# Kernel optimization log

Hardware: AMD Instinct MI355X
Metric: run time of the kernel (lower is better)

Reference implementation:

```python
import jax, jax.numpy as jnp
import numpy as np

EMBED = 1024
HEADS = 16
HEAD_DIM = EMBED // HEADS
B, S = 8, 1024


def setup_inputs() -> dict:
    key = jax.random.key(0)
    ks = jax.random.split(key, 9)
    sd = 0.02
    return {
        "x": jax.random.normal(ks[0], (B, S, EMBED), dtype=jnp.float32),
        "wq": jax.random.normal(ks[1], (EMBED, EMBED), dtype=jnp.float32) * sd,
        "bq": jnp.zeros((EMBED,), dtype=jnp.float32),
        "wk": jax.random.normal(ks[2], (EMBED, EMBED), dtype=jnp.float32) * sd,
        "bk": jnp.zeros((EMBED,), dtype=jnp.float32),
        "wv": jax.random.normal(ks[3], (EMBED, EMBED), dtype=jnp.float32) * sd,
        "bv": jnp.zeros((EMBED,), dtype=jnp.float32),
        "wo": jax.random.normal(ks[4], (EMBED, EMBED), dtype=jnp.float32) * sd,
        "bo": jnp.zeros((EMBED,), dtype=jnp.float32),
    }


def reference(x, wq, bq, wk, bk, wv, bv, wo, bo):
    b, s, e = x.shape
    scale = HEAD_DIM ** -0.5
    # projections (torch Linear: x @ W^T + b)
    q = x @ wq.T + bq
    k = x @ wk.T + bk
    v = x @ wv.T + bv
    # [b, h, s, d]
    q = q.reshape(b, s, HEADS, HEAD_DIM).transpose(0, 2, 1, 3)
    k = k.reshape(b, s, HEADS, HEAD_DIM).transpose(0, 2, 1, 3)
    v = v.reshape(b, s, HEADS, HEAD_DIM).transpose(0, 2, 1, 3)
    scores = jnp.einsum("bhqd,bhkd->bhqk", q, k) * scale
    probs = jax.nn.softmax(scores, axis=-1)
    out = jnp.einsum("bhqk,bhkd->bhqd", probs, v)
    out = out.transpose(0, 2, 1, 3).reshape(b, s, e)
    return out @ wo.T + bo
```

## Files before the change

### kernel.cpp

```cpp
#include <hip/hip_runtime.h>
#include <hip/hip_bf16.h>
#include <math.h>

#define EMBED 1024
#define HEADS 16
#define HDIM 64
#define BATCH 8
#define SEQL 1024
#define MROWS (BATCH * SEQL)

typedef _Float16 f16x8 __attribute__((ext_vector_type(8)));
typedef float    f32x4 __attribute__((ext_vector_type(4)));

__device__ __forceinline__ void gload_lds16(const void* g, void* l) {
    __builtin_amdgcn_global_load_lds(
        (__attribute__((address_space(1))) void*)g,
        (__attribute__((address_space(3))) void*)l, 16, 0, 0);
}

__device__ __forceinline__ unsigned pack_f16(float a, float b) {
    union { _Float16 h[2]; unsigned u; } t;
    t.h[0] = (_Float16)a; t.h[1] = (_Float16)b;
    return t.u;
}

__global__ __launch_bounds__(256)
void cvt_f16(const float* __restrict__ in, _Float16* __restrict__ out)
{
    const int r = blockIdx.x;
    const int c4 = threadIdx.x * 4;
    const float4 v = *reinterpret_cast<const float4*>(&in[(size_t)r * EMBED + c4]);
    union { _Float16 h[4]; short4 s; } u;
    u.h[0] = (_Float16)v.x; u.h[1] = (_Float16)v.y;
    u.h[2] = (_Float16)v.z; u.h[3] = (_Float16)v.w;
    *reinterpret_cast<short4*>(out + (size_t)r * EMBED + c4) = u.s;
}

__global__ __launch_bounds__(256)
void cvt_w4(const float* __restrict__ wq, const float* __restrict__ wk,
            const float* __restrict__ wv, const float* __restrict__ wo,
            _Float16* __restrict__ out)
{
    const int bid  = blockIdx.x;
    const int wsel = bid >> 10;
    const int row  = bid & 1023;
    const float* in = (wsel == 0) ? wq : (wsel == 1) ? wk : (wsel == 2) ? wv : wo;
    const int c4 = threadIdx.x * 4;
    const float4 v = *reinterpret_cast<const float4*>(&in[(size_t)row * EMBED + c4]);
    union { _Float16 h[4]; short4 s; } u;
    u.h[0] = (_Float16)v.x; u.h[1] = (_Float16)v.y;
    u.h[2] = (_Float16)v.z; u.h[3] = (_Float16)v.w;
    *reinterpret_cast<short4*>(out + (size_t)bid * EMBED + c4) = u.s;
}

#define GN EMBED
#define BK 64

template <int MODE>
__global__ __launch_bounds__(256)
void gemm_mfma(const _Float16* __restrict__ A, const _Float16* __restrict__ B,
               const float* __restrict__ bias, void* __restrict__ Cout,
               float scale)
{
    __shared__ __align__(16) _Float16 As[128][BK];
    __shared__ __align__(16) _Float16 Bs[128][BK];

    const int bid = blockIdx.x;
    const int xcd = bid & 7;
    const int idx = bid >> 3;
    const int bm  = (xcd * 8 + (idx >> 3)) * 128;
    const int bn  = (idx & 7) * 128;

    const int tid = threadIdx.x;
    const int w    = tid >> 6;
    const int lane = tid & 63;
    const int lr = lane & 15;
    const int lh = lane >> 4;
    const int wr = w >> 1;
    const int wc = w & 1;

    f32x4 acc[4][4];
    #pragma unroll
    for (int m = 0; m < 4; ++m)
        #pragma unroll
        for (int n = 0; n < 4; ++n) acc[m][n] = (f32x4){0.f, 0.f, 0.f, 0.f};

    for (int step = 0; step < 16; ++step) {
        const int kbase = step * BK;

        #pragma unroll
        for (int i = 0; i < 4; ++i) {
            const int idx2 = tid + i * 256;
            const int r    = idx2 >> 3;
            const int kc   = (idx2 & 7) * 8;
            gload_lds16(A + (size_t)(bm + r) * EMBED + kbase + kc,
                        (char*)As + i * 4096 + w * 1024);
            gload_lds16(B + (size_t)(bn + r) * EMBED + kbase + kc,
                        (char*)Bs + i * 4096 + w * 1024);
        }
        __syncthreads();

        #pragma unroll
        for (int kk = 0; kk < 2; ++kk) {
            f16x8 af[4], bfr[4];
            #pragma unroll
            for (int m = 0; m < 4; ++m)
                af[m] = *reinterpret_cast<const f16x8*>(
                    &As[wr * 64 + m * 16 + lr][kk * 32 + lh * 8]);
            #pragma unroll
            for (int n = 0; n < 4; ++n)
                bfr[n] = *reinterpret_cast<const f16x8*>(
                    &Bs[wc * 64 + n * 16 + lr][kk * 32 + lh * 8]);
            #pragma unroll
            for (int m = 0; m < 4; ++m)
                #pragma unroll
                for (int n = 0; n < 4; ++n)
                    acc[m][n] = __builtin_amdgcn_mfma_f32_16x16x32_f16(
                        af[m], bfr[n], acc[m][n], 0, 0, 0);
        }
        __syncthreads();
    }

    #pragma unroll
    for (int m = 0; m < 4; ++m) {
        #pragma unroll
        for (int n = 0; n < 4; ++n) {
            const int col = bn + wc * 64 + n * 16 + lr;
            const float bv = bias[col];
            #pragma unroll
            for (int j = 0; j < 4; ++j) {
                const int row = bm + wr * 64 + m * 16 + lh * 4 + j;
                const float f = acc[m][n][j] + bv;
                if (MODE == 0) {
                    ((float*)Cout)[(size_t)row * GN + col] = f;
                } else {
                    const int b = row >> 10, s = row & 1023;
                    const int h = col >> 6,  d = col & 63;
                    if (MODE == 2) {
                        ((_Float16*)Cout)[((size_t)(b * HEADS + h) * HDIM + d) * SEQL + s] =
                            (_Float16)f;
                    } else {
                        ((_Float16*)Cout)[((size_t)(b * HEADS + h) * SEQL + s) * HDIM + d] =
                            (_Float16)(f * scale);
                    }
                }
            }
        }
    }
}

#define KT 64

__global__ __launch_bounds__(512, 8)
void attn_mfma(const _Float16* __restrict__ Q2, const _Float16* __restrict__ K2,
               const _Float16* __restrict__ VT, _Float16* __restrict__ Ab)
{
    __shared__ __align__(16) char KVs[2][2][8192];

    const int bid = blockIdx.x;
    const int xcd = bid & 7;
    const int idx = bid >> 3;
    const int bh  = xcd * 16 + (idx >> 3);
    const int qt0 = (idx & 7) * 128;

    const int tid  = threadIdx.x;
    const int w    = tid >> 6;
    const int lane = tid & 63;
    const int lr = lane & 15;
    const int lh = lane >> 4;
    const int b   = bh >> 4;

    const _Float16* Qg = Q2 + (size_t)bh * SEQL * 64;
    const _Float16* Kg = K2 + (size_t)bh * SEQL * 64;
    const _Float16* Vg = VT + (size_t)bh * HDIM * SEQL;

    f16x8 qf[2];
    {
        const _Float16* qrow = Qg + (size_t)(qt0 + w * 16 + lr) * 64 + lh * 8;
        qf[0] = *reinterpret_cast<const f16x8*>(qrow);
        qf[1] = *reinterpret_cast<const f16x8*>(qrow + 32);
    }

    f32x4 oacc[4];
    #pragma unroll
    for (int nd = 0; nd < 4; ++nd) oacc[nd] = (f32x4){0.f, 0.f, 0.f, 0.f};
    float l_run = 0.f;

    const int s0 = lr + 32 * (lh & 1);
    const int s1 = s0 + 16;
    const bool hi_n = (lh >> 1) != 0;

#define STAGE(bufi, ktv) do {                                                  \
        const int r_  = tid >> 3;                                              \
        const int cb_ = ((tid & 7) * 16) ^ ((r_ & 7) << 4);                    \
        gload_lds16(Kg + (size_t)((ktv) * KT + r_) * 64 + cb_ / 2,             \
                    &KVs[bufi][0][w * 1024]);                                  \
        gload_lds16(Vg + (size_t)r_ * SEQL + (ktv) * KT + cb_ / 2,             \
                    &KVs[bufi][1][w * 1024]);                                  \
    } while (0)

    STAGE(0, 0);
    __syncthreads();

    for (int kt = 0; kt < SEQL / KT; ++kt) {
        if (kt < 15) STAGE((kt + 1) & 1, kt + 1);

        const char* Kb = (const char*)KVs[kt & 1][0];
        const char* Vb = (const char*)KVs[kt & 1][1];

        f32x4 sc[4];
        __builtin_amdgcn_s_setprio(1);
        #pragma unroll
        for (int n = 0; n < 4; ++n) {
            const int row = n * 16 + lr;
            const int o0 = row * 128 + ((lh * 16) ^ ((row & 7) << 4));
            const int o1 = row * 128 + ((64 + lh * 16) ^ ((row & 7) << 4));
            const f16x8 kf0 = *reinterpret_cast<const f16x8*>(Kb + o0);
            const f16x8 kf1 = *reinterpret_cast<const f16x8*>(Kb + o1);
            f32x4 s = (f32x4){0.f, 0.f, 0.f, 0.f};
            s = __builtin_amdgcn_mfma_f32_16x16x32_f16(kf0, qf[0], s, 0, 0, 0);
            s = __builtin_amdgcn_mfma_f32_16x16x32_f16(kf1, qf[1], s, 0, 0, 0);
            sc[n] = s;
        }
        __builtin_amdgcn_s_setprio(0);

        float p[4][4];
        float psn[4];
        #pragma unroll
        for (int n = 0; n < 4; ++n) {
            #pragma unroll
            for (int j = 0; j < 4; ++j)
                p[n][j] = exp2f(sc[n][j]);
            psn[n] = (p[n][0] + p[n][1]) + (p[n][2] + p[n][3]);
        }
        l_run += (psn[0] + psn[1]) + (psn[2] + psn[3]);

        unsigned pk[4][2];
        #pragma unroll
        for (int n = 0; n < 4; ++n) {
            pk[n][0] = pack_f16(p[n][0], p[n][1]);
            pk[n][1] = pack_f16(p[n][2], p[n][3]);
        }

        unsigned pa[2][4];
        #pragma unroll
        for (int ks = 0; ks < 2; ++ks) {
            const unsigned a0 = __shfl(pk[2 * ks][0],     s0);
            const unsigned b0 = __shfl(pk[2 * ks + 1][0], s0);
            const unsigned a1 = __shfl(pk[2 * ks][1],     s0);
            const unsigned b1 = __shfl(pk[2 * ks + 1][1], s0);
            const unsigned a2 = __shfl(pk[2 * ks][0],     s1);
            const unsigned b2 = __shfl(pk[2 * ks + 1][0], s1);
            const unsigned a3 = __shfl(pk[2 * ks][1],     s1);
            const unsigned b3 = __shfl(pk[2 * ks + 1][1], s1);
            pa[ks][0] = hi_n ? b0 : a0;
            pa[ks][1] = hi_n ? b1 : a1;
            pa[ks][2] = hi_n ? b2 : a2;
            pa[ks][3] = hi_n ? b3 : a3;
        }

        __builtin_amdgcn_s_setprio(1);
        #pragma unroll
        for (int ks = 0; ks < 2; ++ks) {
            const f16x8 pf = *reinterpret_cast<const f16x8*>(&pa[ks][0]);
            #pragma unroll
            for (int nd = 0; nd < 4; ++nd) {
                const int row = nd * 16 + lr;
                const int off = row * 128 +
                    ((ks * 64 + lh * 16) ^ ((row & 7) << 4));
                const f16x8 vf = *reinterpret_cast<const f16x8*>(Vb + off);
                oacc[nd] = __builtin_amdgcn_mfma_f32_16x16x32_f16(
                    pf, vf, oacc[nd], 0, 0, 0);
            }
        }
        __builtin_amdgcn_s_setprio(0);

        __syncthreads();
    }
#undef STAGE

    l_run += __shfl_xor(l_run, 16);
    l_run += __shfl_xor(l_run, 32);

    const int h = bh & (HEADS - 1);
    #pragma unroll
    for (int j = 0; j < 4; ++j) {
        const float lv = __shfl(l_run, (lane & 48) | ((4 * lh + j) & 15));
        const float rl = 1.f / lv;
        const size_t gm = (size_t)b * SEQL + qt0 + w * 16 + 4 * lh + j;
        #pragma unroll
        for (int nd = 0; nd < 4; ++nd) {
            const int e = h * 64 + nd * 16 + lr;
            Ab[gm * EMBED + e] = (_Float16)(oacc[nd][j] * rl);
        }
    }
}

extern "C" void kernel_launch(void* const* d_in, const int* in_sizes, int n_in,
                              void* d_out, int out_size, void* d_ws, size_t ws_size,
                              hipStream_t stream)
{
    const float* x  = (const float*)d_in[0];
    const float* wq = (const float*)d_in[1];
    const float* bq = (const float*)d_in[2];
    const float* wk = (const float*)d_in[3];
    const float* bk = (const float*)d_in[4];
    const float* wv = (const float*)d_in[5];
    const float* bv = (const float*)d_in[6];
    const float* wo = (const float*)d_in[7];
    const float* bo = (const float*)d_in[8];
    float* out = (float*)d_out;

    char* p = (char*)d_ws;
    _Float16* x2  = (_Float16*)p;  p += (size_t)MROWS * EMBED * 2;
    _Float16* wq2 = (_Float16*)p;  p += (size_t)EMBED * EMBED * 2;
    _Float16* wk2 = (_Float16*)p;  p += (size_t)EMBED * EMBED * 2;
    _Float16* wv2 = (_Float16*)p;  p += (size_t)EMBED * EMBED * 2;
    _Float16* wo2 = (_Float16*)p;  p += (size_t)EMBED * EMBED * 2;
    _Float16* Q2  = (_Float16*)p;  p += (size_t)BATCH * HEADS * SEQL * 64 * 2;
    _Float16* K2  = (_Float16*)p;  p += (size_t)BATCH * HEADS * SEQL * 64 * 2;
    _Float16* VT  = (_Float16*)p;  p += (size_t)BATCH * HEADS * HDIM * SEQL * 2;
    _Float16* Ab  = x2;

    const dim3 blk(256);
    cvt_f16<<<dim3(MROWS), blk, 0, stream>>>(x, x2);
    cvt_w4<<<dim3(4096), blk, 0, stream>>>(wq, wk, wv, wo, wq2);

    const float qscale = 0.125f * 1.4426950408889634f;
    gemm_mfma<3><<<dim3(512), blk, 0, stream>>>(x2, wq2, bq, Q2, qscale);
    gemm_mfma<3><<<dim3(512), blk, 0, stream>>>(x2, wk2, bk, K2, 1.0f);
    gemm_mfma<2><<<dim3(512), blk, 0, stream>>>(x2, wv2, bv, VT, 1.0f);

    attn_mfma<<<dim3(1024), dim3(512), 0, stream>>>(Q2, K2, VT, Ab);

    gemm_mfma<0><<<dim3(512), blk, 0, stream>>>(Ab, wo2, bo, out, 1.0f);
}
```

Measured before the change: 196.6 us.

## Fuse Q and K projections into one GEMM and unroll attention loop by two

Q and K projections now run as a single GEMM with N=2048, relying on wq2 and wk2 being contiguous in the workspace, and the epilogue routes columns to the Q or K buffer with per-projection bias and scale. The attention kernel unrolls its K/V loop by two with fixed double-buffer indices, precomputes swizzled LDS offsets and staging pointers outside the loop, and uses the packed cvt_pkrtz instruction for the f16 conversion. The aim is to remove one kernel launch and tail, give the projection GEMM a larger grid, and reduce per-iteration address arithmetic. The packed conversion rounds toward zero instead of to nearest, which slightly changes the probability values.

```diff
diff --git a/kernel.cpp b/kernel.cpp
--- a/kernel.cpp
+++ b/kernel.cpp
@@ -10,6 +10,7 @@
 #define MROWS (BATCH * SEQL)
 
 typedef _Float16 f16x8 __attribute__((ext_vector_type(8)));
+typedef __fp16   fp16x2 __attribute__((ext_vector_type(2)));
 typedef float    f32x4 __attribute__((ext_vector_type(4)));
 
 __device__ __forceinline__ void gload_lds16(const void* g, void* l) {
@@ -19,8 +20,8 @@
 }
 
 __device__ __forceinline__ unsigned pack_f16(float a, float b) {
-    union { _Float16 h[2]; unsigned u; } t;
-    t.h[0] = (_Float16)a; t.h[1] = (_Float16)b;
+    union { fp16x2 h; unsigned u; } t;
+    t.h = __builtin_amdgcn_cvt_pkrtz(a, b);
     return t.u;
 }
 
@@ -56,11 +57,11 @@
 #define GN EMBED
 #define BK 64
 
-template <int MODE>
+template <int MODE, int NBLK>
 __global__ __launch_bounds__(256)
 void gemm_mfma(const _Float16* __restrict__ A, const _Float16* __restrict__ B,
-               const float* __restrict__ bias, void* __restrict__ Cout,
-               float scale)
+               const float* __restrict__ bias, const float* __restrict__ bias2,
+               void* __restrict__ Cout, float scale)
 {
     __shared__ __align__(16) _Float16 As[128][BK];
     __shared__ __align__(16) _Float16 Bs[128][BK];
@@ -68,8 +69,8 @@
     const int bid = blockIdx.x;
     const int xcd = bid & 7;
     const int idx = bid >> 3;
-    const int bm  = (xcd * 8 + (idx >> 3)) * 128;
-    const int bn  = (idx & 7) * 128;
+    const int bm  = (xcd * 8 + (idx / NBLK)) * 128;
+    const int bn  = (idx % NBLK) * 128;
 
     const int tid = threadIdx.x;
     const int w    = tid >> 6;
@@ -126,7 +127,9 @@
         #pragma unroll
         for (int n = 0; n < 4; ++n) {
             const int col = bn + wc * 64 + n * 16 + lr;
-            const float bv = bias[col];
+            const int c   = col & 1023;
+            const int proj = col >> 10;
+            const float bv = (MODE == 4 && proj) ? bias2[c] : bias[c];
             #pragma unroll
             for (int j = 0; j < 4; ++j) {
                 const int row = bm + wr * 64 + m * 16 + lh * 4 + j;
@@ -135,13 +138,15 @@
                     ((float*)Cout)[(size_t)row * GN + col] = f;
                 } else {
                     const int b = row >> 10, s = row & 1023;
-                    const int h = col >> 6,  d = col & 63;
+                    const int h = c >> 6,  d = c & 63;
                     if (MODE == 2) {
                         ((_Float16*)Cout)[((size_t)(b * HEADS + h) * HDIM + d) * SEQL + s] =
                             (_Float16)f;
                     } else {
-                        ((_Float16*)Cout)[((size_t)(b * HEADS + h) * SEQL + s) * HDIM + d] =
-                            (_Float16)(f * scale);
+                        const float sc_ = proj ? 1.0f : scale;
+                        ((_Float16*)Cout)[(size_t)proj * MROWS * EMBED +
+                            ((size_t)(b * HEADS + h) * SEQL + s) * 64 + d] =
+                            (_Float16)(f * sc_);
                     }
                 }
             }
@@ -171,8 +176,11 @@
     const int b   = bh >> 4;
 
     const _Float16* Qg = Q2 + (size_t)bh * SEQL * 64;
-    const _Float16* Kg = K2 + (size_t)bh * SEQL * 64;
-    const _Float16* Vg = VT + (size_t)bh * HDIM * SEQL;
+
+    const int sr  = tid >> 3;
+    const int scb = ((tid & 7) * 16) ^ ((sr & 7) << 4);
+    const _Float16* KgT = K2 + (size_t)bh * SEQL * 64 + (size_t)sr * 64 + scb / 2;
+    const _Float16* VgT = VT + (size_t)bh * HDIM * SEQL + (size_t)sr * SEQL + scb / 2;
 
     f16x8 qf[2];
     {
@@ -181,6 +189,21 @@
         qf[1] = *reinterpret_cast<const f16x8*>(qrow + 32);
     }
 
+    int qk_o0[4], qk_o1[4], pv_o[2][4];
+    #pragma unroll
+    for (int n = 0; n < 4; ++n) {
+        const int row = n * 16 + lr;
+        qk_o0[n] = row * 128 + ((lh * 16) ^ ((row & 7) << 4));
+        qk_o1[n] = row * 128 + ((64 + lh * 16) ^ ((row & 7) << 4));
+    }
+    #pragma unroll
+    for (int ks = 0; ks < 2; ++ks)
+        #pragma unroll
+        for (int nd = 0; nd < 4; ++nd) {
+            const int row = nd * 16 + lr;
+            pv_o[ks][nd] = row * 128 + ((ks * 64 + lh * 16) ^ ((row & 7) << 4));
+        }
+
     f32x4 oacc[4];
     #pragma unroll
     for (int nd = 0; nd < 4; ++nd) oacc[nd] = (f32x4){0.f, 0.f, 0.f, 0.f};
@@ -191,93 +214,84 @@
     const bool hi_n = (lh >> 1) != 0;
 
 #define STAGE(bufi, ktv) do {                                                  \
-        const int r_  = tid >> 3;                                              \
-        const int cb_ = ((tid & 7) * 16) ^ ((r_ & 7) << 4);                    \
-        gload_lds16(Kg + (size_t)((ktv) * KT + r_) * 64 + cb_ / 2,             \
-                    &KVs[bufi][0][w * 1024]);                                  \
-        gload_lds16(Vg + (size_t)r_ * SEQL + (ktv) * KT + cb_ / 2,             \
-                    &KVs[bufi][1][w * 1024]);                                  \
+        gload_lds16(KgT + (ktv) * (KT * 64), &KVs[bufi][0][w * 1024]);         \
+        gload_lds16(VgT + (ktv) * KT,        &KVs[bufi][1][w * 1024]);         \
+    } while (0)
+
+#define TILE(BUF) do {                                                         \
+        const char* Kb_ = (const char*)KVs[BUF][0];                            \
+        const char* Vb_ = (const char*)KVs[BUF][1];                            \
+        f32x4 sc[4];                                                           \
+        __builtin_amdgcn_s_setprio(1);                                         \
+        _Pragma("unroll")                                                      \
+        for (int n = 0; n < 4; ++n) {                                          \
+            const f16x8 kf0 = *reinterpret_cast<const f16x8*>(Kb_ + qk_o0[n]); \
+            const f16x8 kf1 = *reinterpret_cast<const f16x8*>(Kb_ + qk_o1[n]); \
+            f32x4 s_ = (f32x4){0.f, 0.f, 0.f, 0.f};                            \
+            s_ = __builtin_amdgcn_mfma_f32_16x16x32_f16(kf0, qf[0], s_, 0,0,0);\
+            s_ = __builtin_amdgcn_mfma_f32_16x16x32_f16(kf1, qf[1], s_, 0,0,0);\
+            sc[n] = s_;                                                        \
+        }                                                                      \
+        __builtin_amdgcn_s_setprio(0);                                         \
+        float p[4][4]; float psn[4];                                           \
+        _Pragma("unroll")                                                      \
+        for (int n = 0; n < 4; ++n) {                                          \
+            _Pragma("unroll")                                                  \
+            for (int j = 0; j < 4; ++j) p[n][j] = exp2f(sc[n][j]);             \
+            psn[n] = (p[n][0] + p[n][1]) + (p[n][2] + p[n][3]);                \
+        }                                                                      \
+        l_run += (psn[0] + psn[1]) + (psn[2] + psn[3]);                        \
+        unsigned pk[4][2];                                                     \
+        _Pragma("unroll")                                                      \
+        for (int n = 0; n < 4; ++n) {                                          \
+            pk[n][0] = pack_f16(p[n][0], p[n][1]);                             \
+            pk[n][1] = pack_f16(p[n][2], p[n][3]);                             \
+        }                                                                      \
+        unsigned pa[2][4];                                                     \
+        _Pragma("unroll")                                                      \
+        for (int ks = 0; ks < 2; ++ks) {                                       \
+            const unsigned a0 = __shfl(pk[2 * ks][0],     s0);                 \
+            const unsigned b0 = __shfl(pk[2 * ks + 1][0], s0);                 \
+            const unsigned a1 = __shfl(pk[2 * ks][1],     s0);                 \
+            const unsigned b1 = __shfl(pk[2 * ks + 1][1], s0);                 \
+            const unsigned a2 = __shfl(pk[2 * ks][0],     s1);                 \
+            const unsigned b2 = __shfl(pk[2 * ks + 1][0], s1);                 \
+            const unsigned a3 = __shfl(pk[2 * ks][1],     s1);                 \
+            const unsigned b3 = __shfl(pk[2 * ks + 1][1], s1);                 \
+            pa[ks][0] = hi_n ? b0 : a0;                                        \
+            pa[ks][1] = hi_n ? b1 : a1;                                        \
+            pa[ks][2] = hi_n ? b2 : a2;                                        \
+            pa[ks][3] = hi_n ? b3 : a3;                                        \
+        }                                                                      \
+        __builtin_amdgcn_s_setprio(1);                                         \
+        _Pragma("unroll")                                                      \
+        for (int ks = 0; ks < 2; ++ks) {                                       \
+            const f16x8 pf = *reinterpret_cast<const f16x8*>(&pa[ks][0]);      \
+            _Pragma("unroll")                                                  \
+            for (int nd = 0; nd < 4; ++nd) {                                   \
+                const f16x8 vf = *reinterpret_cast<const f16x8*>(              \
+                    Vb_ + pv_o[ks][nd]);                                       \
+                oacc[nd] = __builtin_amdgcn_mfma_f32_16x16x32_f16(             \
+                    pf, vf, oacc[nd], 0, 0, 0);                                \
+            }                                                                  \
+        }                                                                      \
+        __builtin_amdgcn_s_setprio(0);                                         \
     } while (0)
 
     STAGE(0, 0);
     __syncthreads();
 
-    for (int kt = 0; kt < SEQL / KT; ++kt) {
-        if (kt < 15) STAGE((kt + 1) & 1, kt + 1);
-
-        const char* Kb = (const char*)KVs[kt & 1][0];
-        const char* Vb = (const char*)KVs[kt & 1][1];
-
-        f32x4 sc[4];
-        __builtin_amdgcn_s_setprio(1);
-        #pragma unroll
-        for (int n = 0; n < 4; ++n) {
-            const int row = n * 16 + lr;
-            const int o0 = row * 128 + ((lh * 16) ^ ((row & 7) << 4));
-            const int o1 = row * 128 + ((64 + lh * 16) ^ ((row & 7) << 4));
-            const f16x8 kf0 = *reinterpret_cast<const f16x8*>(Kb + o0);
-            const f16x8 kf1 = *reinterpret_cast<const f16x8*>(Kb + o1);
-            f32x4 s = (f32x4){0.f, 0.f, 0.f, 0.f};
-            s = __builtin_amdgcn_mfma_f32_16x16x32_f16(kf0, qf[0], s, 0, 0, 0);
-            s = __builtin_amdgcn_mfma_f32_16x16x32_f16(kf1, qf[1], s, 0, 0, 0);
-            sc[n] = s;
-        }
-        __builtin_amdgcn_s_setprio(0);
-
-        float p[4][4];
-        float psn[4];
-        #pragma unroll
-        for (int n = 0; n < 4; ++n) {
-            #pragma unroll
-            for (int j = 0; j < 4; ++j)
-                p[n][j] = exp2f(sc[n][j]);
-            psn[n] = (p[n][0] + p[n][1]) + (p[n][2] + p[n][3]);
-        }
-        l_run += (psn[0] + psn[1]) + (psn[2] + psn[3]);
-
-        unsigned pk[4][2];
-        #pragma unroll
-        for (int n = 0; n < 4; ++n) {
-            pk[n][0] = pack_f16(p[n][0], p[n][1]);
-            pk[n][1] = pack_f16(p[n][2], p[n][3]);
-        }
-
-        unsigned pa[2][4];
-        #pragma unroll
-        for (int ks = 0; ks < 2; ++ks) {
-            const unsigned a0 = __shfl(pk[2 * ks][0],     s0);
-            const unsigned b0 = __shfl(pk[2 * ks + 1][0], s0);
-            const unsigned a1 = __shfl(pk[2 * ks][1],     s0);
-            const unsigned b1 = __shfl(pk[2 * ks + 1][1], s0);
-            const unsigned a2 = __shfl(pk[2 * ks][0],     s1);
-            const unsigned b2 = __shfl(pk[2 * ks + 1][0], s1);
-            const unsigned a3 = __shfl(pk[2 * ks][1],     s1);
-            const unsigned b3 = __shfl(pk[2 * ks + 1][1], s1);
-            pa[ks][0] = hi_n ? b0 : a0;
-            pa[ks][1] = hi_n ? b1 : a1;
-            pa[ks][2] = hi_n ? b2 : a2;
-            pa[ks][3] = hi_n ? b3 : a3;
-        }
-
-        __builtin_amdgcn_s_setprio(1);
-        #pragma unroll
-        for (int ks = 0; ks < 2; ++ks) {
-            const f16x8 pf = *reinterpret_cast<const f16x8*>(&pa[ks][0]);
-            #pragma unroll
-            for (int nd = 0; nd < 4; ++nd) {
-                const int row = nd * 16 + lr;
-                const int off = row * 128 +
-                    ((ks * 64 + lh * 16) ^ ((row & 7) << 4));
-                const f16x8 vf = *reinterpret_cast<const f16x8*>(Vb + off);
-                oacc[nd] = __builtin_amdgcn_mfma_f32_16x16x32_f16(
-                    pf, vf, oacc[nd], 0, 0, 0);
-            }
-        }
-        __builtin_amdgcn_s_setprio(0);
-
+    #pragma unroll 1
+    for (int kt = 0; kt < SEQL / KT; kt += 2) {
+        STAGE(1, kt + 1);
+        TILE(0);
         __syncthreads();
+        if (kt < 14) STAGE(0, kt + 2);
+        TILE(1);
+        __syncthreads();
     }
 #undef STAGE
+#undef TILE
 
     l_run += __shfl_xor(l_run, 16);
     l_run += __shfl_xor(l_run, 32);
@@ -317,21 +331,21 @@
     _Float16* wk2 = (_Float16*)p;  p += (size_t)EMBED * EMBED * 2;
     _Float16* wv2 = (_Float16*)p;  p += (size_t)EMBED * EMBED * 2;
     _Float16* wo2 = (_Float16*)p;  p += (size_t)EMBED * EMBED * 2;
-    _Float16* Q2  = (_Float16*)p;  p += (size_t)BATCH * HEADS * SEQL * 64 * 2;
-    _Float16* K2  = (_Float16*)p;  p += (size_t)BATCH * HEADS * SEQL * 64 * 2;
-    _Float16* VT  = (_Float16*)p;  p += (size_t)BATCH * HEADS * HDIM * SEQL * 2;
+    _Float16* Q2  = (_Float16*)p;  p += (size_t)MROWS * EMBED * 2;
+    _Float16* K2  = (_Float16*)p;  p += (size_t)MROWS * EMBED * 2;
+    _Float16* VT  = (_Float16*)p;  p += (size_t)MROWS * EMBED * 2;
     _Float16* Ab  = x2;
+    (void)wk2; (void)n_in; (void)in_sizes; (void)out_size; (void)ws_size;
 
     const dim3 blk(256);
     cvt_f16<<<dim3(MROWS), blk, 0, stream>>>(x, x2);
     cvt_w4<<<dim3(4096), blk, 0, stream>>>(wq, wk, wv, wo, wq2);
 
     const float qscale = 0.125f * 1.4426950408889634f;
-    gemm_mfma<3><<<dim3(512), blk, 0, stream>>>(x2, wq2, bq, Q2, qscale);
-    gemm_mfma<3><<<dim3(512), blk, 0, stream>>>(x2, wk2, bk, K2, 1.0f);
-    gemm_mfma<2><<<dim3(512), blk, 0, stream>>>(x2, wv2, bv, VT, 1.0f);
+    gemm_mfma<4, 16><<<dim3(1024), blk, 0, stream>>>(x2, wq2, bq, bk, Q2, qscale);
+    gemm_mfma<2, 8><<<dim3(512),  blk, 0, stream>>>(x2, wv2, bv, bv, VT, 1.0f);
 
     attn_mfma<<<dim3(1024), dim3(512), 0, stream>>>(Q2, K2, VT, Ab);
 
-    gemm_mfma<0><<<dim3(512), blk, 0, stream>>>(Ab, wo2, bo, out, 1.0f);
-}
+    gemm_mfma<0, 8><<<dim3(512), blk, 0, stream>>>(Ab, wo2, bo, bo, out, 1.0f);
+}
```

New measurement: 231.6 us. 17.8% more time.
